# Optimization experiments

Hardware: AMD Instinct MI355X
Metric: run time of the kernel (lower is better)

The kernel has to match this reference:

```python
import jax, jax.numpy as jnp
import numpy as np

B, N, E, H, EXP = 16, 1024, 768, 8, 2
D = E // H
HID = EXP * E
SCALE = 1.0 / (E ** 0.5)  # module divides by e**0.5, not d_head**0.5
EPS = 1e-5


def layer_norm(x, g, b):
    m = jnp.mean(x, axis=-1, keepdims=True)
    v = jnp.var(x, axis=-1, keepdims=True)
    return (x - m) * jax.lax.rsqrt(v + EPS) * g + b


def setup_inputs() -> dict:
    key = jax.random.key(0)
    ks = jax.random.split(key, 8)
    s = lambda fan_in: 1.0 / np.sqrt(fan_in)
    return {
        "x": jax.random.normal(ks[0], (B, N, E), jnp.float32),
        "ln1_g": jnp.ones((E,), jnp.float32),
        "ln1_b": jnp.zeros((E,), jnp.float32),
        "qkv_w": jax.random.normal(ks[1], (E, 3 * E), jnp.float32) * s(E),
        "qkv_b": jnp.zeros((3 * E,), jnp.float32),
        "proj_w": jax.random.normal(ks[2], (E, E), jnp.float32) * s(E),
        "proj_b": jnp.zeros((E,), jnp.float32),
        "ln2_g": jnp.ones((E,), jnp.float32),
        "ln2_b": jnp.zeros((E,), jnp.float32),
        "ff1_w": jax.random.normal(ks[3], (E, HID), jnp.float32) * s(E),
        "ff1_b": jnp.zeros((HID,), jnp.float32),
        "ff2_w": jax.random.normal(ks[4], (HID, E), jnp.float32) * s(HID),
        "ff2_b": jnp.zeros((E,), jnp.float32),
    }


def reference(x, ln1_g, ln1_b, qkv_w, qkv_b, proj_w, proj_b,
              ln2_g, ln2_b, ff1_w, ff1_b, ff2_w, ff2_b):
    b, n, e = x.shape
    # --- attention sub-block (pre-norm, residual) ---
    h = layer_norm(x, ln1_g, ln1_b)
    qkv = h @ qkv_w + qkv_b                       # [b, n, 3e]
    # einops 'b n (h d t) -> t b h n d'
    qkv = qkv.reshape(b, n, H, D, 3)
    q = jnp.transpose(qkv[..., 0], (0, 2, 1, 3))   # [b, h, n, d]
    k = jnp.transpose(qkv[..., 1], (0, 2, 1, 3))
    v = jnp.transpose(qkv[..., 2], (0, 2, 1, 3))
    att = jax.nn.softmax(jnp.einsum('bhnd,bhmd->bhnm', q, k) * SCALE, axis=-1)
    out = jnp.einsum('bhnm,bhmd->bhnd', att, v)    # [b, h, n, d]
    out = jnp.transpose(out, (0, 2, 1, 3)).reshape(b, n, e)
    x = x + (out @ proj_w + proj_b)
    # --- FFN sub-block (pre-norm, residual) ---
    h = layer_norm(x, ln2_g, ln2_b)
    h = jax.nn.gelu(h @ ff1_w + ff1_b, approximate=False)
    x = x + (h @ ff2_w + ff2_b)
    return x
```

## Files before the change

### kernel.cpp

```cpp
#include <hip/hip_runtime.h>
#include <hip/hip_bf16.h>
#include <cstddef>

#define B_   16
#define N_   1024
#define E_   768
#define H_   8
#define D_   96
#define HID_ 1536
#define ROWS (B_ * N_)
#define SCALE_  0.03608439182435161f
#define QSCALE_ 0.052058774f

typedef __attribute__((ext_vector_type(8))) short bf16x8;
typedef __attribute__((ext_vector_type(4))) float f32x4;

__device__ __forceinline__ unsigned short f2bf(float f) {
    union { float f; unsigned int u; } c; c.f = f;
    unsigned int u = c.u + 0x7FFFu + ((c.u >> 16) & 1u);
    return (unsigned short)(u >> 16);
}

__device__ __forceinline__ unsigned short f2bf_hw(float f) {
    union { __hip_bfloat16 h; unsigned short u; } c;
    c.h = __float2bfloat16(f);
    return c.u;
}

__device__ __forceinline__ void gload16(const void* g, void* l) {
    __builtin_amdgcn_global_load_lds(
        (const __attribute__((address_space(1))) unsigned int*)g,
        (__attribute__((address_space(3))) unsigned int*)l, 16, 0, 0);
}

__device__ __forceinline__ float gelu_exact(float x) {
    return 0.5f * x * (1.0f + erff(x * 0.7071067811865475f));
}

__global__ __launch_bounds__(256) void wcvt_kernel(const float* __restrict__ W,
                                                   unsigned short* __restrict__ Wt,
                                                   int K, int N) {
    __shared__ float t[32][33];
    int n0 = blockIdx.x * 32, k0 = blockIdx.y * 32;
    int tr = threadIdx.x >> 3;
    int tc = (threadIdx.x & 7) * 4;
    float4 v = *(const float4*)&W[(size_t)(k0 + tr) * N + n0 + tc];
    t[tr][tc + 0] = v.x; t[tr][tc + 1] = v.y; t[tr][tc + 2] = v.z; t[tr][tc + 3] = v.w;
    __syncthreads();
    ushort4 o;
    o.x = f2bf(t[tc + 0][tr]);
    o.y = f2bf(t[tc + 1][tr]);
    o.z = f2bf(t[tc + 2][tr]);
    o.w = f2bf(t[tc + 3][tr]);
    *(ushort4*)&Wt[(size_t)(n0 + tr) * K + k0 + tc] = o;
}

__global__ __launch_bounds__(256) void ln_fused_kernel(const float* __restrict__ x,
                                                       const float* __restrict__ g,
                                                       const float* __restrict__ beta,
                                                       unsigned short* __restrict__ out) {
    int row = blockIdx.x;
    int tid = threadIdx.x;
    const float* xr = x + (size_t)row * E_;
    float v0 = xr[tid];
    float v1 = xr[tid + 256];
    float v2 = xr[tid + 512];
    float s  = v0 + v1 + v2;
    float s2 = v0 * v0 + v1 * v1 + v2 * v2;
#pragma unroll
    for (int off = 32; off > 0; off >>= 1) {
        s  += __shfl_down(s, off);
        s2 += __shfl_down(s2, off);
    }
    __shared__ float sb[8];
    __shared__ float stats[2];
    int lane = tid & 63, wid = tid >> 6;
    if (lane == 0) { sb[wid] = s; sb[4 + wid] = s2; }
    __syncthreads();
    if (tid == 0) {
        float S  = sb[0] + sb[1] + sb[2] + sb[3];
        float S2 = sb[4] + sb[5] + sb[6] + sb[7];
        float m = S * (1.0f / E_);
        float var = S2 * (1.0f / E_) - m * m;
        stats[0] = m;
        stats[1] = rsqrtf(var + 1e-5f);
    }
    __syncthreads();
    float mean = stats[0], rstd = stats[1];
    unsigned short* orow = out + (size_t)row * E_;
    orow[tid]       = f2bf((v0 - mean) * rstd * g[tid]       + beta[tid]);
    orow[tid + 256] = f2bf((v1 - mean) * rstd * g[tid + 256] + beta[tid + 256]);
    orow[tid + 512] = f2bf((v2 - mean) * rstd * g[tid + 512] + beta[tid + 512]);
}

template<int MODE>
__global__ __launch_bounds__(256) void bgemm_kernel(
    const unsigned short* __restrict__ A, const unsigned short* __restrict__ Wt,
    const float* __restrict__ bias,
    const float* R, float* C, unsigned short* Cb,
    unsigned short* qo, unsigned short* ko, unsigned short* vo,
    int M, int N, int K)
{
    __shared__ __align__(16) unsigned short As[128 * 32];
    __shared__ __align__(16) unsigned short Bs[128 * 32];
    const int tid = threadIdx.x;
    const int l = tid & 63, w = tid >> 6;
    const int bm = blockIdx.y * 128, bn = blockIdx.x * 128;
    const int wr = (w >> 1) * 64, wc = (w & 1) * 64;
    const int l15 = l & 15, l4 = l >> 4;

    const int srow = w * 16 + (l >> 2);
    const int scol = (l & 3) * 8;
    const unsigned short* Ag = A  + (size_t)(bm + srow) * K + scol;
    const unsigned short* Wg = Wt + (size_t)(bn + srow) * K + scol;
    unsigned short* AsW = As + w * 512;
    unsigned short* BsW = Bs + w * 512;

    f32x4 acc[4][4] = {};

    for (int k0 = 0; k0 < K; k0 += 32) {
        __syncthreads();
        gload16(Ag + k0,                  AsW);
        gload16(Ag + (size_t)64 * K + k0, AsW + 2048);
        gload16(Wg + k0,                  BsW);
        gload16(Wg + (size_t)64 * K + k0, BsW + 2048);
        __syncthreads();
        bf16x8 af[4], bfr[4];
#pragma unroll
        for (int mi = 0; mi < 4; ++mi)
            af[mi] = *(const bf16x8*)&As[(wr + mi * 16 + l15) * 32 + l4 * 8];
#pragma unroll
        for (int ni = 0; ni < 4; ++ni)
            bfr[ni] = *(const bf16x8*)&Bs[(wc + ni * 16 + l15) * 32 + l4 * 8];
#pragma unroll
        for (int mi = 0; mi < 4; ++mi)
#pragma unroll
            for (int ni = 0; ni < 4; ++ni)
                acc[mi][ni] = __builtin_amdgcn_mfma_f32_16x16x32_bf16(
                    af[mi], bfr[ni], acc[mi][ni], 0, 0, 0);
    }

    const int r0 = bm + wr + l4 * 4;
    const int c0 = bn + wc + l15;
    float bv[4];
#pragma unroll
    for (int ni = 0; ni < 4; ++ni) bv[ni] = bias[c0 + ni * 16];

#pragma unroll
    for (int mi = 0; mi < 4; ++mi) {
#pragma unroll
        for (int r = 0; r < 4; ++r) {
            int row = r0 + mi * 16 + r;
            if constexpr (MODE == 0) {
                size_t base = (size_t)row * N;
#pragma unroll
                for (int ni = 0; ni < 4; ++ni) {
                    size_t idx = base + c0 + ni * 16;
                    C[idx] = acc[mi][ni][r] + bv[ni] + R[idx];
                }
            } else if constexpr (MODE == 1) {
                size_t base = (size_t)row * N;
#pragma unroll
                for (int ni = 0; ni < 4; ++ni) {
                    size_t idx = base + c0 + ni * 16;
                    Cb[idx] = f2bf(gelu_exact(acc[mi][ni][r] + bv[ni]));
                }
            } else {
                int b = row >> 10, ntok = row & (N_ - 1);
#pragma unroll
                for (int ni = 0; ni < 4; ++ni) {
                    int n = c0 + ni * 16;
                    int e = n / 3, t = n - e * 3;
                    int hh = e / D_, dd = e - hh * D_;
                    float cval = acc[mi][ni][r] + bv[ni];
                    size_t bh = (size_t)(b * H_ + hh);
                    if (t == 0)      qo[(bh * N_ + ntok) * D_ + dd] = f2bf(cval * QSCALE_);
                    else if (t == 1) ko[(bh * N_ + ntok) * D_ + dd] = f2bf(cval);
                    else             vo[(bh * D_ + dd) * N_ + ntok] = f2bf(cval);
                }
            }
        }
    }
}

#define QT  64
#define KVT 64
#define NT  (N_ / KVT)

__global__ __launch_bounds__(256) void fattn_kernel(
    const unsigned short* __restrict__ qg, const unsigned short* __restrict__ kg,
    const unsigned short* __restrict__ vtg, unsigned short* __restrict__ out) {
    int bh = blockIdx.y;
    int b = bh >> 3, h = bh & 7;
    int q0 = blockIdx.x * QT;
    int tid = threadIdx.x;
    int l = tid & 63, w = tid >> 6;
    int q16 = l & 15, g = l >> 4;
    int hi2 = (l >> 5) & 1;
    const int swz = (q16 & 7) << 3;

    __shared__ __align__(16) unsigned short Qs[QT * D_];
    __shared__ __align__(16) unsigned short Ks[KVT * D_];
    __shared__ __align__(16) unsigned short Vts[D_ * KVT];

    const int krow = tid >> 2, kc8 = (tid & 3) * 24;
    const int ksw = (krow & 7) << 3;
    const int vrow0 = tid >> 3, vc8 = (tid & 7) * 8;

    {
        const uint4* src = (const uint4*)(qg + ((size_t)bh * N_ + q0 + krow) * D_ + kc8);
#pragma unroll
        for (int i = 0; i < 3; ++i)
            *(uint4*)&Qs[(krow * D_ + kc8 + i * 8) ^ ksw] = src[i];
    }
    __syncthreads();

    bf16x8 qf[3];
#pragma unroll
    for (int dc = 0; dc < 3; ++dc)
        qf[dc] = *(const bf16x8*)&Qs[((w * 16 + q16) * D_ + dc * 32 + g * 8) ^ swz];

    float m_run = -INFINITY, l_run = 0.f;
    f32x4 oacc[6] = {};

    for (int kt = 0; kt < NT; ++kt) {
        __syncthreads();
        {
            const uint4* ks = (const uint4*)(kg + ((size_t)bh * N_ + kt * KVT + krow) * D_ + kc8);
#pragma unroll
            for (int i = 0; i < 3; ++i)
                *(uint4*)&Ks[(krow * D_ + kc8 + i * 8) ^ ksw] = ks[i];
#pragma unroll
            for (int p = 0; p < 3; ++p) {
                int row = vrow0 + p * 32;
                *(uint4*)&Vts[(row * KVT + vc8) ^ ((row & 7) << 3)] =
                    *(const uint4*)(vtg + ((size_t)bh * D_ + row) * N_ + kt * KVT + vc8);
            }
        }
        __syncthreads();

        f32x4 sacc[4] = {};
#pragma unroll
        for (int sub = 0; sub < 4; ++sub)
#pragma unroll
            for (int dc = 0; dc < 3; ++dc) {
                bf16x8 af = *(const bf16x8*)&Ks[((sub * 16 + q16) * D_ + dc * 32 + g * 8) ^ swz];
                sacc[sub] = __builtin_amdgcn_mfma_f32_16x16x32_bf16(af, qf[dc], sacc[sub], 0, 0, 0);
            }

        float pmax = -INFINITY;
#pragma unroll
        for (int s = 0; s < 4; ++s)
#pragma unroll
            for (int r = 0; r < 4; ++r) pmax = fmaxf(pmax, sacc[s][r]);
        pmax = fmaxf(pmax, __shfl_xor(pmax, 16));
        pmax = fmaxf(pmax, __shfl_xor(pmax, 32));
        if (!__all(pmax - m_run <= 11.0f)) {
            float m_new = fmaxf(m_run, pmax);
            float fac = exp2f(m_run - m_new);
#pragma unroll
            for (int d = 0; d < 6; ++d)
#pragma unroll
                for (int r = 0; r < 4; ++r) oacc[d][r] *= fac;
            l_run *= fac;
            m_run = m_new;
        }
        float pe[4][4];
        float rs = 0.f;
#pragma unroll
        for (int s = 0; s < 4; ++s)
#pragma unroll
            for (int r = 0; r < 4; ++r) {
                pe[s][r] = exp2f(sacc[s][r] - m_run);
                rs += pe[s][r];
            }
        rs += __shfl_xor(rs, 16);
        rs += __shfl_xor(rs, 32);
        l_run += rs;

        unsigned int pk[4][2];
#pragma unroll
        for (int s = 0; s < 4; ++s)
#pragma unroll
            for (int j = 0; j < 2; ++j)
                pk[s][j] = (unsigned)f2bf_hw(pe[s][2 * j]) |
                           ((unsigned)f2bf_hw(pe[s][2 * j + 1]) << 16);
        union { unsigned int u[4]; bf16x8 v; } pfu[2];
#pragma unroll
        for (int c = 0; c < 2; ++c)
#pragma unroll
            for (int j = 0; j < 4; ++j) {
                int gsrc = (g & 1) * 2 + (j >> 1);
                int src = q16 + (gsrc << 4);
                unsigned a = (unsigned)__shfl((int)pk[c * 2][j & 1], src);
                unsigned bb = (unsigned)__shfl((int)pk[c * 2 + 1][j & 1], src);
                pfu[c].u[j] = hi2 ? bb : a;
            }

#pragma unroll
        for (int dsub = 0; dsub < 6; ++dsub)
#pragma unroll
            for (int c = 0; c < 2; ++c) {
                bf16x8 vf = *(const bf16x8*)&Vts[((dsub * 16 + q16) * KVT + c * 32 + g * 8) ^ swz];
                oacc[dsub] = __builtin_amdgcn_mfma_f32_16x16x32_bf16(vf, pfu[c].v, oacc[dsub], 0, 0, 0);
            }
    }

    float inv = 1.0f / l_run;
    int qrow = q0 + w * 16 + q16;
    size_t base = ((size_t)(b * N_ + qrow)) * E_ + h * D_;
#pragma unroll
    for (int dsub = 0; dsub < 6; ++dsub)
#pragma unroll
        for (int r = 0; r < 4; ++r)
            out[base + dsub * 16 + g * 4 + r] = f2bf_hw(oacc[dsub][r] * inv);
}

extern "C" void kernel_launch(void* const* d_in, const int* in_sizes, int n_in,
                              void* d_out, int out_size, void* d_ws, size_t ws_size,
                              hipStream_t stream) {
    const float* x      = (const float*)d_in[0];
    const float* ln1_g  = (const float*)d_in[1];
    const float* ln1_b  = (const float*)d_in[2];
    const float* qkv_w  = (const float*)d_in[3];
    const float* qkv_b  = (const float*)d_in[4];
    const float* proj_w = (const float*)d_in[5];
    const float* proj_b = (const float*)d_in[6];
    const float* ln2_g  = (const float*)d_in[7];
    const float* ln2_b  = (const float*)d_in[8];
    const float* ff1_w  = (const float*)d_in[9];
    const float* ff1_b  = (const float*)d_in[10];
    const float* ff2_w  = (const float*)d_in[11];
    const float* ff2_b  = (const float*)d_in[12];
    float* out = (float*)d_out;
    float* ws  = (float*)d_ws;

    const size_t S = (size_t)ROWS * E_ / 2;
    unsigned short* qkv_wt = (unsigned short*)ws;
    unsigned short* proj_wt = qkv_wt + (size_t)3 * E_ * E_;
    unsigned short* ff1_wt  = proj_wt + (size_t)E_ * E_;
    unsigned short* ff2_wt  = ff1_wt + (size_t)HID_ * E_;
    float* Rb = ws + 2359296;
    unsigned short* h16   = (unsigned short*)(Rb);
    unsigned short* q16   = (unsigned short*)(Rb + S);
    unsigned short* k16   = (unsigned short*)(Rb + 2 * S);
    unsigned short* vt16  = (unsigned short*)(Rb + 3 * S);
    unsigned short* attnb = h16;
    unsigned short* h16b  = q16;
    unsigned short* ffh   = k16;
    float* x1 = out;

    wcvt_kernel<<<dim3(3 * E_ / 32, E_ / 32), 256, 0, stream>>>(qkv_w, qkv_wt, E_, 3 * E_);
    wcvt_kernel<<<dim3(E_ / 32, E_ / 32), 256, 0, stream>>>(proj_w, proj_wt, E_, E_);
    wcvt_kernel<<<dim3(HID_ / 32, E_ / 32), 256, 0, stream>>>(ff1_w, ff1_wt, E_, HID_);
    wcvt_kernel<<<dim3(E_ / 32, HID_ / 32), 256, 0, stream>>>(ff2_w, ff2_wt, HID_, E_);
    ln_fused_kernel<<<ROWS, 256, 0, stream>>>(x, ln1_g, ln1_b, h16);
    bgemm_kernel<2><<<dim3(3 * E_ / 128, ROWS / 128), 256, 0, stream>>>(
        h16, qkv_wt, qkv_b, nullptr, nullptr, nullptr, q16, k16, vt16,
        ROWS, 3 * E_, E_);
    fattn_kernel<<<dim3(N_ / QT, B_ * H_), 256, 0, stream>>>(q16, k16, vt16, attnb);
    bgemm_kernel<0><<<dim3(E_ / 128, ROWS / 128), 256, 0, stream>>>(
        attnb, proj_wt, proj_b, x, x1, nullptr, nullptr, nullptr, nullptr,
        ROWS, E_, E_);
    ln_fused_kernel<<<ROWS, 256, 0, stream>>>(x1, ln2_g, ln2_b, h16b);
    bgemm_kernel<1><<<dim3(HID_ / 128, ROWS / 128), 256, 0, stream>>>(
        h16b, ff1_wt, ff1_b, nullptr, nullptr, ffh, nullptr, nullptr, nullptr,
        ROWS, HID_, E_);
    bgemm_kernel<0><<<dim3(E_ / 128, ROWS / 128), 256, 0, stream>>>(
        ffh, ff2_wt, ff2_b, x1, out, nullptr, nullptr, nullptr, nullptr,
        ROWS, E_, HID_);
}
```

Measured before the change: 623.4 us.

## Use direct-to-LDS loads in attention, swizzle GEMM block order, set MFMA priority

The attention kernel now loads K and V^T tiles straight into shared memory with gload16 (global-to-LDS) instead of staging them through registers. K rows are padded to 128 elements and XOR-swizzled so the reads stay conflict-free. The GEMM remaps block indices so that consecutive blocks are spread in groups of eight, which is meant to improve L2/XCD locality. The QKV epilogue index math is hoisted out of the row loop, and s_setprio is raised around the MFMA sections. The padding increases LDS use, and the remap assumes the grid size divides by eight.

```diff
diff --git a/kernel.cpp b/kernel.cpp
--- a/kernel.cpp
+++ b/kernel.cpp
@@ -105,7 +105,11 @@
     __shared__ __align__(16) unsigned short Bs[128 * 32];
     const int tid = threadIdx.x;
     const int l = tid & 63, w = tid >> 6;
-    const int bm = blockIdx.y * 128, bn = blockIdx.x * 128;
+    const int NXg = gridDim.x;
+    const int flat = blockIdx.y * NXg + blockIdx.x;
+    const int cpx = (NXg * gridDim.y) >> 3;
+    const int wid2 = (flat & 7) * cpx + (flat >> 3);
+    const int bm = (wid2 / NXg) * 128, bn = (wid2 % NXg) * 128;
     const int wr = (w >> 1) * 64, wc = (w & 1) * 64;
     const int l15 = l & 15, l4 = l >> 4;
 
@@ -146,6 +150,16 @@
 #pragma unroll
     for (int ni = 0; ni < 4; ++ni) bv[ni] = bias[c0 + ni * 16];
 
+    int e4[4], t4[4], hh4[4], dd4[4];
+    if constexpr (MODE == 2) {
+#pragma unroll
+        for (int ni = 0; ni < 4; ++ni) {
+            int n = c0 + ni * 16;
+            e4[ni] = n / 3; t4[ni] = n - e4[ni] * 3;
+            hh4[ni] = e4[ni] / D_; dd4[ni] = e4[ni] - hh4[ni] * D_;
+        }
+    }
+
 #pragma unroll
     for (int mi = 0; mi < 4; ++mi) {
 #pragma unroll
@@ -169,14 +183,11 @@
                 int b = row >> 10, ntok = row & (N_ - 1);
 #pragma unroll
                 for (int ni = 0; ni < 4; ++ni) {
-                    int n = c0 + ni * 16;
-                    int e = n / 3, t = n - e * 3;
-                    int hh = e / D_, dd = e - hh * D_;
                     float cval = acc[mi][ni][r] + bv[ni];
-                    size_t bh = (size_t)(b * H_ + hh);
-                    if (t == 0)      qo[(bh * N_ + ntok) * D_ + dd] = f2bf(cval * QSCALE_);
-                    else if (t == 1) ko[(bh * N_ + ntok) * D_ + dd] = f2bf(cval);
-                    else             vo[(bh * D_ + dd) * N_ + ntok] = f2bf(cval);
+                    size_t bh = (size_t)(b * H_ + hh4[ni]);
+                    if (t4[ni] == 0)      qo[(bh * N_ + ntok) * D_ + dd4[ni]] = f2bf(cval * QSCALE_);
+                    else if (t4[ni] == 1) ko[(bh * N_ + ntok) * D_ + dd4[ni]] = f2bf(cval);
+                    else                  vo[(bh * D_ + dd4[ni]) * N_ + ntok] = f2bf(cval);
                 }
             }
         }
@@ -200,19 +211,36 @@
     const int swz = (q16 & 7) << 3;
 
     __shared__ __align__(16) unsigned short Qs[QT * D_];
-    __shared__ __align__(16) unsigned short Ks[KVT * D_];
+    __shared__ __align__(16) unsigned short Ks[KVT * 128];
     __shared__ __align__(16) unsigned short Vts[D_ * KVT];
 
-    const int krow = tid >> 2, kc8 = (tid & 3) * 24;
-    const int ksw = (krow & 7) << 3;
-    const int vrow0 = tid >> 3, vc8 = (tid & 7) * 8;
-
     {
+        int krow = tid >> 2, kc8 = (tid & 3) * 24;
+        int ksw = (krow & 7) << 3;
         const uint4* src = (const uint4*)(qg + ((size_t)bh * N_ + q0 + krow) * D_ + kc8);
 #pragma unroll
         for (int i = 0; i < 3; ++i)
             *(uint4*)&Qs[(krow * D_ + kc8 + i * 8) ^ ksw] = src[i];
     }
+
+    const unsigned short* kbase[4];
+#pragma unroll
+    for (int i = 0; i < 4; ++i) {
+        int r = w * 4 + i;
+        int rowK = r * 4 + (l >> 4);
+        int c8 = (l & 15) ^ (rowK & 7);
+        if (c8 >= 12) c8 = 0;
+        kbase[i] = kg + ((size_t)bh * N_ + rowK) * D_ + c8 * 8;
+    }
+    const unsigned short* vbase[3];
+#pragma unroll
+    for (int i = 0; i < 3; ++i) {
+        int r = w * 3 + i;
+        int rowV = r * 8 + (l >> 3);
+        int c8 = (l & 7) ^ (rowV & 7);
+        vbase[i] = vtg + ((size_t)bh * D_ + rowV) * N_ + c8 * 8;
+    }
+
     __syncthreads();
 
     bf16x8 qf[3];
@@ -225,28 +253,25 @@
 
     for (int kt = 0; kt < NT; ++kt) {
         __syncthreads();
-        {
-            const uint4* ks = (const uint4*)(kg + ((size_t)bh * N_ + kt * KVT + krow) * D_ + kc8);
-#pragma unroll
-            for (int i = 0; i < 3; ++i)
-                *(uint4*)&Ks[(krow * D_ + kc8 + i * 8) ^ ksw] = ks[i];
-#pragma unroll
-            for (int p = 0; p < 3; ++p) {
-                int row = vrow0 + p * 32;
-                *(uint4*)&Vts[(row * KVT + vc8) ^ ((row & 7) << 3)] =
-                    *(const uint4*)(vtg + ((size_t)bh * D_ + row) * N_ + kt * KVT + vc8);
-            }
-        }
+#pragma unroll
+        for (int i = 0; i < 4; ++i)
+            gload16(kbase[i] + (size_t)kt * KVT * D_, Ks + (w * 4 + i) * 512);
+#pragma unroll
+        for (int i = 0; i < 3; ++i)
+            gload16(vbase[i] + (size_t)kt * KVT, Vts + (w * 3 + i) * 512);
         __syncthreads();
 
         f32x4 sacc[4] = {};
+        __builtin_amdgcn_s_setprio(1);
 #pragma unroll
         for (int sub = 0; sub < 4; ++sub)
 #pragma unroll
             for (int dc = 0; dc < 3; ++dc) {
-                bf16x8 af = *(const bf16x8*)&Ks[((sub * 16 + q16) * D_ + dc * 32 + g * 8) ^ swz];
+                bf16x8 af = *(const bf16x8*)&Ks[(sub * 16 + q16) * 128 +
+                                                (((dc << 2) + g) ^ (q16 & 7)) * 8];
                 sacc[sub] = __builtin_amdgcn_mfma_f32_16x16x32_bf16(af, qf[dc], sacc[sub], 0, 0, 0);
             }
+        __builtin_amdgcn_s_setprio(0);
 
         float pmax = -INFINITY;
 #pragma unroll
@@ -297,6 +322,7 @@
                 pfu[c].u[j] = hi2 ? bb : a;
             }
 
+        __builtin_amdgcn_s_setprio(1);
 #pragma unroll
         for (int dsub = 0; dsub < 6; ++dsub)
 #pragma unroll
@@ -304,6 +330,7 @@
                 bf16x8 vf = *(const bf16x8*)&Vts[((dsub * 16 + q16) * KVT + c * 32 + g * 8) ^ swz];
                 oacc[dsub] = __builtin_amdgcn_mfma_f32_16x16x32_bf16(vf, pfu[c].v, oacc[dsub], 0, 0, 0);
             }
+        __builtin_amdgcn_s_setprio(0);
     }
 
     float inv = 1.0f / l_run;
```

After: 580.5 us. -6.9%, faster.
